# Kernel tuning notes

Hardware: AMD Instinct MI355X
Metric: run time of the kernel (lower is better)

The kernel has to match this reference:

```python
import jax, jax.numpy as jnp
import numpy as np
from jax import lax

N_NODES = 200000
FEAT = 64
B = 4096
DEG = 32
P = 2048
EMBED = 64
CONTRA = 64
EPS = 1e-8


def _cos(a, b):
    # cosine similarity along last axis, torch-style eps clamp
    num = jnp.sum(a * b, axis=-1)
    na = jnp.sqrt(jnp.sum(a * a, axis=-1))
    nb = jnp.sqrt(jnp.sum(b * b, axis=-1))
    return num / (jnp.maximum(na, EPS) * jnp.maximum(nb, EPS))


def setup_inputs() -> dict:
    key = jax.random.key(0)
    ks = jax.random.split(key, 16)
    return {
        "nodes": jax.random.randint(ks[0], (B,), 0, N_NODES),
        "labels": jax.random.randint(ks[1], (B,), 0, 2),
        "neigh1": jax.random.randint(ks[2], (B, DEG), 0, N_NODES),
        "neigh2": jax.random.randint(ks[3], (B, DEG), 0, N_NODES),
        "neigh3": jax.random.randint(ks[4], (B, DEG), 0, N_NODES),
        "pos_nodes": jax.random.randint(ks[5], (P,), 0, N_NODES),
        "features": jax.random.normal(ks[6], (N_NODES, FEAT), jnp.float32),
        "weight": jax.random.normal(ks[7], (EMBED * 3 + FEAT, EMBED), jnp.float32) * 0.05,
        "rsimTrans": jax.random.normal(ks[8], (FEAT, CONTRA), jnp.float32) * 0.05,
        "pos_embs": jax.random.normal(ks[9], (3, CONTRA), jnp.float32),
        "W1": jax.random.normal(ks[10], (FEAT, EMBED), jnp.float32) * 0.05,
        "W2": jax.random.normal(ks[11], (FEAT, EMBED), jnp.float32) * 0.05,
        "W3": jax.random.normal(ks[12], (FEAT, EMBED), jnp.float32) * 0.05,
        "sample_num": 16,
    }


def _relation(features, rsimTrans, center_orig, center_sim, pos_sim, neigh, pos_emb, W, sample_num):
    n_orig = features[neigh]                               # [B, D, F] irregular gather
    n_sim = jax.nn.relu(jnp.einsum('bdf,fc->bdc', n_orig, rsimTrans))  # [B, D, C]
    neigh_scores = _cos(center_orig[:, None, :], n_orig)   # [B, D]
    neigh_pos_scores = _cos(pos_emb[None, None, :], n_sim) # [B, D]
    pos_scores = _cos(pos_emb[None, :], pos_sim)           # [P]
    center_scores = _cos(pos_emb[None, :], center_sim)     # [B]
    # per-relation sampling: keep top ceil(D*rho) neighbors by pos-similarity
    _, idx = lax.top_k(neigh_pos_scores, sample_num)       # [B, k]
    sampled = jnp.take_along_axis(n_orig, idx[..., None], axis=1)  # [B, k, F]
    agg = jnp.mean(sampled, axis=1)                        # [B, F]
    r_feats = jax.nn.relu(agg @ W)                         # [B, E]
    sampled_pos = jnp.take_along_axis(neigh_pos_scores, idx, axis=1)
    loss = jnp.mean((sampled_pos - jnp.mean(pos_scores)) ** 2)
    return r_feats, loss


def reference(nodes, labels, neigh1, neigh2, neigh3, pos_nodes, features,
              weight, rsimTrans, pos_embs, W1, W2, W3, sample_num):
    center_orig = features[nodes]                              # [B, F]
    center_sim = jax.nn.relu(center_orig @ rsimTrans)          # [B, C]
    pos_sim = jax.nn.relu(features[pos_nodes] @ rsimTrans)     # [P, C]

    r1, l1 = _relation(features, rsimTrans, center_orig, center_sim, pos_sim,
                       neigh1, pos_embs[0], W1, sample_num)
    r2, l2 = _relation(features, rsimTrans, center_orig, center_sim, pos_sim,
                       neigh2, pos_embs[1], W2, sample_num)
    r3, l3 = _relation(features, rsimTrans, center_orig, center_sim, pos_sim,
                       neigh3, pos_embs[2], W3, sample_num)

    cat_feats = jnp.concatenate([center_orig, r1, r2, r3], axis=1)  # [B, F+3E]
    combined = jax.nn.relu(cat_feats @ weight).T                    # [E, B]
    feat_contra_loss = (l1 + l2 + l3) / 3.0
    return combined, feat_contra_loss
```

## Files before the change

kernel.cpp:

```cpp
#include <hip/hip_runtime.h>
#include <hip/hip_bf16.h>

#define NN     200000
#define FEATD  64
#define BN     4096
#define DEG    32
#define PP     2048
#define EMB    64
#define EPSV   1e-8f
#define NTILE64 3125
#define AWAVES  2048

#define WS_SC    0
#define WS_MISC  800000
#define WS_LOSS  800064
#define WS_RF    800832

typedef short  bf16x8 __attribute__((ext_vector_type(8)));
typedef float  f32x4  __attribute__((ext_vector_type(4)));

__device__ __forceinline__ unsigned int bfr(float x) {
    unsigned int u = __float_as_uint(x);
    return (u + 0x7FFFu + ((u >> 16) & 1u)) & 0xFFFF0000u;
}

__global__ __launch_bounds__(256, 2) void node_precompute(
    const float* __restrict__ features, const float* __restrict__ rsim,
    const float* __restrict__ pos_embs, float4* __restrict__ node_sc)
{
    __shared__ unsigned int lds[4][2][8][64][4];
    int t = threadIdx.x, w = t >> 6, l = t & 63;
    int lg = l >> 4;
    int lr = l & 15;
    const float4* Gf = (const float4*)features;

    bf16x8 rhi[2][4], rlo[2][4];
#pragma unroll
    for (int kk = 0; kk < 2; ++kk)
#pragma unroll
        for (int nf = 0; nf < 4; ++nf) {
            union { unsigned int u[4]; bf16x8 v; } H, L;
#pragma unroll
            for (int i = 0; i < 4; ++i) {
                int k0 = kk * 32 + lg * 8 + i * 2;
                int j  = nf * 16 + lr;
                float x0 = rsim[k0 * 64 + j];
                float x1 = rsim[(k0 + 1) * 64 + j];
                unsigned int r0 = bfr(x0), r1 = bfr(x1);
                H.u[i] = (r0 >> 16) | r1;
                float l0 = x0 - __uint_as_float(r0);
                float l1 = x1 - __uint_as_float(r1);
                L.u[i] = (__float_as_uint(l0) >> 16)
                       | (__float_as_uint(l1) & 0xFFFF0000u);
            }
            rhi[kk][nf] = H.v; rlo[kk][nf] = L.v;
        }

    float pe[3][4];
#pragma unroll
    for (int rr = 0; rr < 3; ++rr)
#pragma unroll
        for (int nf = 0; nf < 4; ++nf)
            pe[rr][nf] = pos_embs[rr * 64 + nf * 16 + lr];

    unsigned int (*Lhi)[64][4] = lds[w][0];
    unsigned int (*Llo)[64][4] = lds[w][1];

    for (int tile = blockIdx.x * 4 + w; tile < NTILE64; tile += AWAVES) {
        const float4* src = Gf + (size_t)tile * 1024;

#pragma unroll
        for (int s = 0; s < 16; ++s) {
            float4 v = src[s * 64 + l];
            int node = s * 4 + lg;
            int kg = lr >> 1, half = lr & 1;
            unsigned int rx = bfr(v.x), ry = bfr(v.y);
            unsigned int rz = bfr(v.z), rw = bfr(v.w);
            unsigned int h0 = (rx >> 16) | ry;
            unsigned int h1 = (rz >> 16) | rw;
            float lx = v.x - __uint_as_float(rx), ly = v.y - __uint_as_float(ry);
            float lz = v.z - __uint_as_float(rz), lw = v.w - __uint_as_float(rw);
            unsigned int l0 = (__float_as_uint(lx) >> 16)
                            | (__float_as_uint(ly) & 0xFFFF0000u);
            unsigned int l1 = (__float_as_uint(lz) >> 16)
                            | (__float_as_uint(lw) & 0xFFFF0000u);
            uint2* dh = (uint2*)&Lhi[kg][node ^ kg][half * 2];
            uint2* dl = (uint2*)&Llo[kg][node ^ kg][half * 2];
            *dh = make_uint2(h0, h1);
            *dl = make_uint2(l0, l1);
        }

        const bf16x8* ph = (const bf16x8*)Lhi;
        const bf16x8* pl = (const bf16x8*)Llo;

#pragma unroll
        for (int mf = 0; mf < 4; ++mf) {
            int node = mf * 16 + lr;
            bf16x8 ah0 = ph[lg * 64 + (node ^ lg)];
            bf16x8 ah1 = ph[(4 + lg) * 64 + (node ^ (4 + lg))];
            bf16x8 al0 = pl[lg * 64 + (node ^ lg)];
            bf16x8 al1 = pl[(4 + lg) * 64 + (node ^ (4 + lg))];

            f32x4 acc[4];
#pragma unroll
            for (int nf = 0; nf < 4; ++nf) acc[nf] = (f32x4)(0.f);
#pragma unroll
            for (int nf = 0; nf < 4; ++nf) {
                acc[nf] = __builtin_amdgcn_mfma_f32_16x16x32_bf16(
                              ah0, rhi[0][nf], acc[nf], 0, 0, 0);
                acc[nf] = __builtin_amdgcn_mfma_f32_16x16x32_bf16(
                              ah1, rhi[1][nf], acc[nf], 0, 0, 0);
                acc[nf] = __builtin_amdgcn_mfma_f32_16x16x32_bf16(
                              ah0, rlo[0][nf], acc[nf], 0, 0, 0);
                acc[nf] = __builtin_amdgcn_mfma_f32_16x16x32_bf16(
                              ah1, rlo[1][nf], acc[nf], 0, 0, 0);
                acc[nf] = __builtin_amdgcn_mfma_f32_16x16x32_bf16(
                              al0, rhi[0][nf], acc[nf], 0, 0, 0);
                acc[nf] = __builtin_amdgcn_mfma_f32_16x16x32_bf16(
                              al1, rhi[1][nf], acc[nf], 0, 0, 0);
            }

            float q[4] = {0,0,0,0}, s0[4] = {0,0,0,0};
            float s1[4] = {0,0,0,0}, s2[4] = {0,0,0,0};
#pragma unroll
            for (int reg = 0; reg < 4; ++reg)
#pragma unroll
                for (int nf = 0; nf < 4; ++nf) {
                    float v = fmaxf(acc[nf][reg], 0.f);
                    q[reg]  += v * v;
                    s0[reg] += v * pe[0][nf];
                    s1[reg] += v * pe[1][nf];
                    s2[reg] += v * pe[2][nf];
                }
#pragma unroll
            for (int o = 1; o < 16; o <<= 1)
#pragma unroll
                for (int reg = 0; reg < 4; ++reg) {
                    q[reg]  += __shfl_xor(q[reg],  o);
                    s0[reg] += __shfl_xor(s0[reg], o);
                    s1[reg] += __shfl_xor(s1[reg], o);
                    s2[reg] += __shfl_xor(s2[reg], o);
                }
            if (lr < 4) {
                int r = l & 3;
                float o0 = (r==0)?s0[0]:(r==1)?s0[1]:(r==2)?s0[2]:s0[3];
                float o1 = (r==0)?s1[0]:(r==1)?s1[1]:(r==2)?s1[2]:s1[3];
                float o2 = (r==0)?s2[0]:(r==1)?s2[1]:(r==2)?s2[2]:s2[3];
                float oq = (r==0)?q[0] :(r==1)?q[1] :(r==2)?q[2] :q[3];
                int n = tile * 64 + mf * 16 + lg * 4 + r;
                node_sc[n] = make_float4(o0, o1, o2, sqrtf(oq));
            }
        }
    }
}

__global__ __launch_bounds__(1024) void pos_stats(
    const int* __restrict__ pos_nodes, const float4* __restrict__ node_sc,
    const float* __restrict__ pos_embs, float* __restrict__ misc,
    float* __restrict__ lossacc)
{
    __shared__ float invpe_s[3];
    __shared__ float wsum[16][3];
    int t = threadIdx.x, wv = t >> 6, lane = t & 63;

    if (t < 24) lossacc[t * 32] = 0.f;

    float pv = (t < 192) ? pos_embs[t] : 0.f;
    float q = pv * pv;
#pragma unroll
    for (int off = 32; off; off >>= 1) q += __shfl_down(q, off);
    if (t < 192 && lane == 0) {
        float inv = 1.f / fmaxf(sqrtf(q), EPSV);
        invpe_s[wv] = inv;
        misc[4 + wv] = inv;
    }
    __syncthreads();

    float i0 = invpe_s[0], i1 = invpe_s[1], i2 = invpe_s[2];
    float s0 = 0.f, s1 = 0.f, s2 = 0.f;
    for (int p = t; p < PP; p += 1024) {
        int n = pos_nodes[p];
        float4 sc = node_sc[n];
        float invn = 1.f / fmaxf(sc.w, EPSV);
        s0 += sc.x * i0 * invn;
        s1 += sc.y * i1 * invn;
        s2 += sc.z * i2 * invn;
    }
#pragma unroll
    for (int off = 32; off; off >>= 1) {
        s0 += __shfl_down(s0, off);
        s1 += __shfl_down(s1, off);
        s2 += __shfl_down(s2, off);
    }
    if (lane == 0) { wsum[wv][0] = s0; wsum[wv][1] = s1; wsum[wv][2] = s2; }
    __syncthreads();
    if (t < 3) {
        float s = 0.f;
        for (int w = 0; w < 16; ++w) s += wsum[w][t];
        misc[t] = s / (float)PP;
    }
}

__global__ __launch_bounds__(256) void relation_agg(
    const int* __restrict__ n1, const int* __restrict__ n2, const int* __restrict__ n3,
    const float* __restrict__ features, const float4* __restrict__ node_sc,
    const float* __restrict__ W1, const float* __restrict__ W2, const float* __restrict__ W3,
    const float* __restrict__ misc, float* __restrict__ lossacc,
    float* __restrict__ rfeat, const int* __restrict__ smp)
{
    int r = blockIdx.y;
    const int*   neigh = (r == 0) ? n1 : (r == 1) ? n2 : n3;
    const float* W     = (r == 0) ? W1 : (r == 1) ? W2 : W3;
    int k = smp[0];
    int t = threadIdx.x;
    int wv = t >> 6, lane = t & 63;
    int b = blockIdx.x * 4 + wv;
    float inv_pe   = misc[4 + r];
    float mean_pos = misc[r];

    __shared__ int sel_ids[4][32];
    __shared__ float4 aggl[4][16];

    float s = -1e30f;
    int   n = 0;
    if (lane < 32) {
        n = neigh[b * DEG + lane];
        float4 sc = node_sc[n];
        float num = (r == 0) ? sc.x : (r == 1) ? sc.y : sc.z;
        s = num * inv_pe / fmaxf(sc.w, EPSV);
    }
    int cnt = 0;
#pragma unroll
    for (int d2 = 0; d2 < 32; ++d2) {
        float v = __shfl(s, d2);
        cnt += ((v > s) || (v == s && d2 < lane)) ? 1 : 0;
    }
    bool sel = (lane < 32) && (cnt < k);
    if (sel) sel_ids[wv][cnt] = n;

    float lv = sel ? (s - mean_pos) * (s - mean_pos) : 0.f;
#pragma unroll
    for (int off = 32; off; off >>= 1) lv += __shfl_down(lv, off);
    if (lane == 0)
        atomicAdd(&lossacc[(r * 8 + (blockIdx.x & 7)) * 32], lv);

    const float4* F = (const float4*)features;
    int col   = lane & 15;
    int rbase = lane >> 4;
    float4 a = make_float4(0.f, 0.f, 0.f, 0.f);
    if (k == 16) {
        int nid0 = sel_ids[wv][rbase];
        int nid1 = sel_ids[wv][rbase + 4];
        int nid2 = sel_ids[wv][rbase + 8];
        int nid3 = sel_ids[wv][rbase + 12];
        float4 v0 = F[(size_t)nid0 * 16 + col];
        float4 v1 = F[(size_t)nid1 * 16 + col];
        float4 v2 = F[(size_t)nid2 * 16 + col];
        float4 v3 = F[(size_t)nid3 * 16 + col];
        a.x = v0.x + v1.x + v2.x + v3.x;
        a.y = v0.y + v1.y + v2.y + v3.y;
        a.z = v0.z + v1.z + v2.z + v3.z;
        a.w = v0.w + v1.w + v2.w + v3.w;
    } else {
        for (int row0 = 0; row0 < k; row0 += 4) {
            int row = row0 + rbase;
            if (row < k) {
                int nid = sel_ids[wv][row];
                float4 v = F[(size_t)nid * 16 + col];
                a.x += v.x; a.y += v.y; a.z += v.z; a.w += v.w;
            }
        }
    }
#pragma unroll
    for (int off = 16; off <= 32; off <<= 1) {
        a.x += __shfl_xor(a.x, off);
        a.y += __shfl_xor(a.y, off);
        a.z += __shfl_xor(a.z, off);
        a.w += __shfl_xor(a.w, off);
    }
    float inv_k = 1.f / (float)k;
    a.x *= inv_k; a.y *= inv_k; a.z *= inv_k; a.w *= inv_k;

    if (lane < 16) aggl[wv][lane] = a;

    float acc = 0.f;
#pragma unroll
    for (int j4 = 0; j4 < 16; ++j4) {
        float4 ag = aggl[wv][j4];
        acc += ag.x * W[(j4 * 4 + 0) * EMB + lane]
             + ag.y * W[(j4 * 4 + 1) * EMB + lane]
             + ag.z * W[(j4 * 4 + 2) * EMB + lane]
             + ag.w * W[(j4 * 4 + 3) * EMB + lane];
    }
    rfeat[((size_t)r * BN + b) * EMB + lane] = fmaxf(acc, 0.f);
}

#define CSTRIDE 264
__global__ __launch_bounds__(256) void final_mm(
    const int* __restrict__ nodes, const float* __restrict__ features,
    const float* __restrict__ rfeat, const float* __restrict__ weight,
    const float* __restrict__ lossacc, const int* __restrict__ smp,
    float* __restrict__ out)
{
    __shared__ float cat_b[8 * CSTRIDE];
    __shared__ float trans[8 * 65];
    __shared__ float ls[24];
    int t = threadIdx.x;
    int b0 = blockIdx.x * 8;

    if (blockIdx.x == 0 && t < 24) ls[t] = lossacc[t * 32];

    for (int idx = t; idx < 512; idx += 256) {
        int bb = idx >> 6, f = idx & 63;
        cat_b[bb * CSTRIDE + f] = features[(size_t)nodes[b0 + bb] * FEATD + f];
    }
#pragma unroll
    for (int r = 0; r < 3; ++r)
        for (int idx = t; idx < 512; idx += 256) {
            int bb = idx >> 6, j = idx & 63;
            cat_b[bb * CSTRIDE + 64 + r * 64 + j] =
                rfeat[((size_t)r * BN + b0 + bb) * EMB + j];
        }
    __syncthreads();

    int wv = t >> 6, lane = t & 63;
    int bb0 = wv * 2;
    float acc0 = 0.f, acc1 = 0.f;
    const float* c0p = &cat_b[bb0 * CSTRIDE];
    const float* c1p = &cat_b[(bb0 + 1) * CSTRIDE];
    for (int i0 = 0; i0 < 256; i0 += 16) {
        float w[16];
#pragma unroll
        for (int u = 0; u < 16; ++u)
            w[u] = weight[(i0 + u) * EMB + lane];
#pragma unroll
        for (int u = 0; u < 16; ++u) {
            acc0 += w[u] * c0p[i0 + u];
            acc1 += w[u] * c1p[i0 + u];
        }
    }
    trans[bb0 * 65 + lane]       = fmaxf(acc0, 0.f);
    trans[(bb0 + 1) * 65 + lane] = fmaxf(acc1, 0.f);
    __syncthreads();

    for (int idx = t; idx < 512; idx += 256) {
        int e = idx >> 3, bb = idx & 7;
        out[(size_t)e * BN + b0 + bb] = trans[bb * 65 + e];
    }

    if (blockIdx.x == 0 && t == 0) {
        int k = smp[0];
        float s = 0.f;
        for (int i = 0; i < 24; ++i) s += ls[i];
        out[(size_t)EMB * BN] = s / (3.f * (float)BN * (float)k);
    }
}

extern "C" void kernel_launch(void* const* d_in, const int* in_sizes, int n_in,
                              void* d_out, int out_size, void* d_ws, size_t ws_size,
                              hipStream_t stream) {
    const int*   nodes     = (const int*)  d_in[0];
    const int*   neigh1    = (const int*)  d_in[2];
    const int*   neigh2    = (const int*)  d_in[3];
    const int*   neigh3    = (const int*)  d_in[4];
    const int*   pos_nodes = (const int*)  d_in[5];
    const float* features  = (const float*)d_in[6];
    const float* weight    = (const float*)d_in[7];
    const float* rsim      = (const float*)d_in[8];
    const float* pos_embs  = (const float*)d_in[9];
    const float* W1        = (const float*)d_in[10];
    const float* W2        = (const float*)d_in[11];
    const float* W3        = (const float*)d_in[12];
    const int*   smp       = (const int*)  d_in[13];
    float* out = (float*)d_out;
    float* ws  = (float*)d_ws;

    float4* node_sc = (float4*)(ws + WS_SC);
    float*  misc    = ws + WS_MISC;
    float*  lossacc = ws + WS_LOSS;
    float*  rfeat   = ws + WS_RF;

    node_precompute<<<dim3(512), dim3(256), 0, stream>>>(
        features, rsim, pos_embs, node_sc);
    pos_stats<<<dim3(1), dim3(1024), 0, stream>>>(
        pos_nodes, node_sc, pos_embs, misc, lossacc);
    relation_agg<<<dim3(BN / 4, 3), dim3(256), 0, stream>>>(
        neigh1, neigh2, neigh3, features, node_sc, W1, W2, W3,
        misc, lossacc, rfeat, smp);
    final_mm<<<dim3(BN / 8), dim3(256), 0, stream>>>(
        nodes, features, rfeat, weight, lossacc, smp, out);
}
```

Before: 70.05 us.

## Prefetch next feature tile into registers and reduce row sums via LDS transpose

The node precompute loop now loads the next tile's features into registers while the current tile's MFMA work runs, so global-load latency overlaps with compute. The per-row reduction over 16 lanes, previously 64 xor-shuffles per fragment, is replaced by writing partial sums to a skewed LDS transpose buffer and then doing a 4-way read plus two shuffle steps. This raises register pressure (16 float4 held across the loop) and adds LDS traffic, which could lower occupancy.

After: 68.26 us. 2.6% less time.

```diff
diff --git a/kernel.cpp b/kernel.cpp
--- a/kernel.cpp
+++ b/kernel.cpp
@@ -29,6 +29,7 @@
     const float* __restrict__ pos_embs, float4* __restrict__ node_sc)
 {
     __shared__ unsigned int lds[4][2][8][64][4];
+    __shared__ float4 trp[4][16][16];
     int t = threadIdx.x, w = t >> 6, l = t & 63;
     int lg = l >> 4;
     int lr = l & 15;
@@ -65,13 +66,20 @@
 
     unsigned int (*Lhi)[64][4] = lds[w][0];
     unsigned int (*Llo)[64][4] = lds[w][1];
-
-    for (int tile = blockIdx.x * 4 + w; tile < NTILE64; tile += AWAVES) {
+    float4 (*T)[16] = trp[w];
+
+    float4 vv[16];
+    int tile = blockIdx.x * 4 + w;
+    if (tile < NTILE64) {
         const float4* src = Gf + (size_t)tile * 1024;
-
+#pragma unroll
+        for (int s = 0; s < 16; ++s) vv[s] = src[s * 64 + l];
+    }
+
+    for (; tile < NTILE64; tile += AWAVES) {
 #pragma unroll
         for (int s = 0; s < 16; ++s) {
-            float4 v = src[s * 64 + l];
+            float4 v = vv[s];
             int node = s * 4 + lg;
             int kg = lr >> 1, half = lr & 1;
             unsigned int rx = bfr(v.x), ry = bfr(v.y);
@@ -90,6 +98,13 @@
             *dl = make_uint2(l0, l1);
         }
 
+        int nt = tile + AWAVES;
+        if (nt < NTILE64) {
+            const float4* src = Gf + (size_t)nt * 1024;
+#pragma unroll
+            for (int s = 0; s < 16; ++s) vv[s] = src[s * 64 + l];
+        }
+
         const bf16x8* ph = (const bf16x8*)Lhi;
         const bf16x8* pl = (const bf16x8*)Llo;
 
@@ -120,36 +135,39 @@
                               al1, rhi[1][nf], acc[nf], 0, 0, 0);
             }
 
-            float q[4] = {0,0,0,0}, s0[4] = {0,0,0,0};
-            float s1[4] = {0,0,0,0}, s2[4] = {0,0,0,0};
-#pragma unroll
-            for (int reg = 0; reg < 4; ++reg)
+#pragma unroll
+            for (int reg = 0; reg < 4; ++reg) {
+                float s0 = 0.f, s1 = 0.f, s2 = 0.f, q = 0.f;
 #pragma unroll
                 for (int nf = 0; nf < 4; ++nf) {
                     float v = fmaxf(acc[nf][reg], 0.f);
-                    q[reg]  += v * v;
-                    s0[reg] += v * pe[0][nf];
-                    s1[reg] += v * pe[1][nf];
-                    s2[reg] += v * pe[2][nf];
+                    s0 += v * pe[0][nf];
+                    s1 += v * pe[1][nf];
+                    s2 += v * pe[2][nf];
+                    q  += v * v;
                 }
-#pragma unroll
-            for (int o = 1; o < 16; o <<= 1)
-#pragma unroll
-                for (int reg = 0; reg < 4; ++reg) {
-                    q[reg]  += __shfl_xor(q[reg],  o);
-                    s0[reg] += __shfl_xor(s0[reg], o);
-                    s1[reg] += __shfl_xor(s1[reg], o);
-                    s2[reg] += __shfl_xor(s2[reg], o);
-                }
-            if (lr < 4) {
-                int r = l & 3;
-                float o0 = (r==0)?s0[0]:(r==1)?s0[1]:(r==2)?s0[2]:s0[3];
-                float o1 = (r==0)?s1[0]:(r==1)?s1[1]:(r==2)?s1[2]:s1[3];
-                float o2 = (r==0)?s2[0]:(r==1)?s2[1]:(r==2)?s2[2]:s2[3];
-                float oq = (r==0)?q[0] :(r==1)?q[1] :(r==2)?q[2] :q[3];
-                int n = tile * 64 + mf * 16 + lg * 4 + r;
-                node_sc[n] = make_float4(o0, o1, o2, sqrtf(oq));
+                int nd = lg * 4 + reg;
+                T[nd][(lr + nd) & 15] = make_float4(s0, s1, s2, q);
             }
+            int rn = l >> 2, rq = l & 3;
+            float4 a0 = T[rn][(rq * 4 + 0 + rn) & 15];
+            float4 a1 = T[rn][(rq * 4 + 1 + rn) & 15];
+            float4 a2 = T[rn][(rq * 4 + 2 + rn) & 15];
+            float4 a3 = T[rn][(rq * 4 + 3 + rn) & 15];
+            float sx = a0.x + a1.x + a2.x + a3.x;
+            float sy = a0.y + a1.y + a2.y + a3.y;
+            float sz = a0.z + a1.z + a2.z + a3.z;
+            float sw = a0.w + a1.w + a2.w + a3.w;
+#pragma unroll
+            for (int o = 1; o < 4; o <<= 1) {
+                sx += __shfl_xor(sx, o);
+                sy += __shfl_xor(sy, o);
+                sz += __shfl_xor(sz, o);
+                sw += __shfl_xor(sw, o);
+            }
+            if (rq == 0)
+                node_sc[tile * 64 + mf * 16 + rn] =
+                    make_float4(sx, sy, sz, sqrtf(sw));
         }
     }
 }
```
